# Performance work log

Measured on AMD Instinct MI355X. Metric: run time of the kernel, lower is better.

## Reference

```python
import jax, jax.numpy as jnp
import numpy as np

B, C, IC, H, W = 2, 64, 32, 96, 96


def setup_inputs() -> dict:
    key = jax.random.key(0)
    ks = jax.random.split(key, 8)
    s_in = 1.0 / np.sqrt(C)
    s_ic = 1.0 / np.sqrt(IC)
    return {
        "x": jax.random.normal(ks[0], (B, C, H, W), dtype=jnp.float32),
        "Wg": jax.random.uniform(ks[1], (IC, C), jnp.float32, -s_in, s_in),
        "bg": jax.random.uniform(ks[2], (IC,), jnp.float32, -s_in, s_in),
        "Wt": jax.random.uniform(ks[3], (IC, C), jnp.float32, -s_in, s_in),
        "bt": jax.random.uniform(ks[4], (IC,), jnp.float32, -s_in, s_in),
        "Wp": jax.random.uniform(ks[5], (IC, C), jnp.float32, -s_in, s_in),
        "bp": jax.random.uniform(ks[6], (IC,), jnp.float32, -s_in, s_in),
        "Wo": jax.random.uniform(ks[7], (C, IC), jnp.float32, -s_ic, s_ic),
        "bo": jax.random.uniform(jax.random.fold_in(key, 9), (C,), jnp.float32, -s_ic, s_ic),
    }


def reference(x, Wg, bg, Wt, bt, Wp, bp, Wo, bo):
    b, c, h, w = x.shape
    n = h * w
    xf = x.reshape(b, c, n)  # [B, C, N]

    def proj(Wc, bc):  # 1x1 conv == channel GEMM -> [B, IC, N]
        return jnp.einsum("bcn,oc->bon", xf, Wc) + bc[None, :, None]

    g = proj(Wg, bg)
    theta = proj(Wt, bt)
    phi = proj(Wp, bp)
    scores = jnp.einsum("bcn,bcm->bnm", theta, phi)  # [B, N, N]
    att = jax.nn.softmax(scores, axis=-1)
    y = jnp.einsum("bnm,bcm->bcn", att, g)  # [B, IC, N]
    o = jnp.einsum("bcn,oc->bon", y, Wo) + bo[None, :, None]  # [B, C, N]
    return o.reshape(b, c, h, w) + x
```

## Files before the change

kernel.cpp:

```cpp
#include <hip/hip_runtime.h>
#include <hip/hip_bf16.h>


#define B_   2
#define C_   64
#define IC_  32
#define N_   9216
#define SEG_       8
#define SEG_KEYS   1152
#define SEG_TILES  18
#define QBLKS      144
#define LOG2E 1.44269504088896f

typedef __attribute__((ext_vector_type(4))) float  f32x4;
typedef __attribute__((ext_vector_type(8))) short  s16x8;
typedef __attribute__((ext_vector_type(4))) short  s16x4;

static __device__ __forceinline__ ushort f2bf(float f) {
  union { __hip_bfloat16 h; ushort u; } cv;
  cv.h = __float2bfloat16(f);
  return cv.u;
}

static __device__ __forceinline__ float bf2f(ushort u) {
  union { uint i; float f; } c;
  c.i = ((uint)u) << 16;
  return c.f;
}

static __device__ __forceinline__ f32x4 mfma32(s16x8 a, s16x8 b, f32x4 c) {
  return __builtin_amdgcn_mfma_f32_16x16x32_bf16(a, b, c, 0, 0, 0);
}

__global__ __launch_bounds__(256) void proj_kernel(
    const float* __restrict__ x,
    const float* __restrict__ Wg, const float* __restrict__ bg,
    const float* __restrict__ Wt, const float* __restrict__ bt,
    const float* __restrict__ Wp, const float* __restrict__ bp,
    ushort* __restrict__ Qb, ushort* __restrict__ Kb, ushort* __restrict__ Vt)
{
  const int g    = blockIdx.x / 18;
  const int nblk = blockIdx.x % 18;
  const int bn0  = nblk * 1024 + threadIdx.x * 4;
  const int b    = bn0 / N_;
  const int n    = bn0 % N_;

  float ag[4], at_[4], ap[4];
#pragma unroll
  for (int j = 0; j < 4; ++j) { ag[j] = 0.f; at_[j] = 0.f; ap[j] = 0.f; }

  const float* xp = x + (size_t)b * C_ * N_ + n;
#pragma unroll 8
  for (int c = 0; c < C_; ++c) {
    const f32x4 x0 = *reinterpret_cast<const f32x4*>(xp + (size_t)c * N_);
    const float wg = Wg[g * C_ + c];
    const float wt = Wt[g * C_ + c];
    const float wp = Wp[g * C_ + c];
#pragma unroll
    for (int j = 0; j < 4; ++j) {
      ag[j]  = fmaf(wg, x0[j], ag[j]);
      at_[j] = fmaf(wt, x0[j], at_[j]);
      ap[j]  = fmaf(wp, x0[j], ap[j]);
    }
  }

  const float bgv = bg[g], btv = bt[g], bpv = bp[g];
  union { ushort u[4]; s16x4 v; } vt4;
#pragma unroll
  for (int j = 0; j < 4; ++j) {
    const int bn = bn0 + j;
    Qb[(size_t)bn * IC_ + g] = f2bf(LOG2E * (at_[j] + btv));
    Kb[(size_t)bn * IC_ + g] = f2bf(ap[j] + bpv);
    vt4.u[j] = f2bf(ag[j] + bgv);
  }
  *reinterpret_cast<s16x4*>(Vt + (size_t)(b * IC_ + g) * N_ + n) = vt4.v;
}

__global__ __launch_bounds__(256) void attn_kernel(
    const ushort* __restrict__ Qb, const ushort* __restrict__ Kb,
    const ushort* __restrict__ Vt, ushort* __restrict__ Opart,
    float* __restrict__ Lp)
{
  __shared__ __align__(16) ushort Kl[64 * 40];
  __shared__ __align__(16) ushort Vl[32 * 68];

  const int qblk = blockIdx.x % QBLKS;
  const int bs   = blockIdx.x / QBLKS;
  const int seg  = bs & (SEG_ - 1);
  const int b    = bs >> 3;
  const int key0 = seg * SEG_KEYS;

  const int tid  = threadIdx.x;
  const int lane = tid & 63;
  const int wave = tid >> 6;
  const int q16  = lane & 15;
  const int h    = lane >> 4;

  const int qbase = qblk * 64 + wave * 16;

  const short ONE = (short)0x3F80;
  const s16x8 ones = {ONE, ONE, ONE, ONE, ONE, ONE, ONE, ONE};

  const s16x8 qfrag = *reinterpret_cast<const s16x8*>(
      Qb + (size_t)(b * N_ + qbase + q16) * IC_ + h * 8);

  f32x4 acc0 = {0.f, 0.f, 0.f, 0.f};
  f32x4 acc1 = {0.f, 0.f, 0.f, 0.f};
  f32x4 accL = {0.f, 0.f, 0.f, 0.f};

  const int krow = tid >> 2, kpart = tid & 3;
  const ushort* kg = Kb + ((size_t)b * N_ + key0 + krow) * IC_ + kpart * 8;
  ushort* kl_dst = &Kl[krow * 40 + kpart * 8];

  const int vd0 = tid >> 4, vp = tid & 15;
  const int vd1 = vd0 + 16;
  const ushort* vg0 = Vt + (size_t)(b * IC_ + vd0) * N_ + key0 + vp * 4;
  const ushort* vg1 = Vt + (size_t)(b * IC_ + vd1) * N_ + key0 + vp * 4;
  ushort* vl_dst0 = &Vl[vd0 * 68 + vp * 4];
  ushort* vl_dst1 = &Vl[vd1 * 68 + vp * 4];

  s16x8 kreg = *reinterpret_cast<const s16x8*>(kg);
  s16x4 vreg0 = *reinterpret_cast<const s16x4*>(vg0);
  s16x4 vreg1 = *reinterpret_cast<const s16x4*>(vg1);

  for (int it = 0; it < SEG_TILES; ++it) {
    *reinterpret_cast<s16x8*>(kl_dst)  = kreg;
    *reinterpret_cast<s16x4*>(vl_dst0) = vreg0;
    *reinterpret_cast<s16x4*>(vl_dst1) = vreg1;
    __syncthreads();

    if (it + 1 < SEG_TILES) {
      const int nk = (it + 1) * 64;
      kreg  = *reinterpret_cast<const s16x8*>(kg + (size_t)nk * IC_);
      vreg0 = *reinterpret_cast<const s16x4*>(vg0 + nk);
      vreg1 = *reinterpret_cast<const s16x4*>(vg1 + nk);
    }

    float sc[4][4];
#pragma unroll
    for (int t = 0; t < 4; ++t) {
      const s16x8 kf = *reinterpret_cast<const s16x8*>(&Kl[(t * 16 + q16) * 40 + h * 8]);
      f32x4 z = {0.f, 0.f, 0.f, 0.f};
      const f32x4 st = mfma32(kf, qfrag, z);
      sc[t][0] = st[0]; sc[t][1] = st[1]; sc[t][2] = st[2]; sc[t][3] = st[3];
    }

#pragma unroll
    for (int u = 0; u < 2; ++u) {
      union { ushort us[8]; s16x8 v; } pa;
#pragma unroll
      for (int i = 0; i < 4; ++i) {
        pa.us[i]     = f2bf(__builtin_amdgcn_exp2f(sc[2 * u][i]));
        pa.us[4 + i] = f2bf(__builtin_amdgcn_exp2f(sc[2 * u + 1][i]));
      }
      union { s16x4 q4[2]; s16x8 v; } vf0, vf1;
      vf0.q4[0] = *reinterpret_cast<const s16x4*>(&Vl[q16 * 68 + u * 32 + h * 4]);
      vf0.q4[1] = *reinterpret_cast<const s16x4*>(&Vl[q16 * 68 + u * 32 + 16 + h * 4]);
      vf1.q4[0] = *reinterpret_cast<const s16x4*>(&Vl[(16 + q16) * 68 + u * 32 + h * 4]);
      vf1.q4[1] = *reinterpret_cast<const s16x4*>(&Vl[(16 + q16) * 68 + u * 32 + 16 + h * 4]);
      acc0 = mfma32(pa.v, vf0.v, acc0);
      acc1 = mfma32(pa.v, vf1.v, acc1);
      accL = mfma32(pa.v, ones,  accL);
    }
    __syncthreads();
  }

  const size_t obase0 = ((size_t)(b * SEG_ + seg) * N_);
#pragma unroll
  for (int r = 0; r < 4; ++r) {
    const int q = qbase + h * 4 + r;
    Opart[(obase0 + q) * IC_ + q16]      = f2bf(acc0[r]);
    Opart[(obase0 + q) * IC_ + 16 + q16] = f2bf(acc1[r]);
  }
  if (q16 == 0) {
#pragma unroll
    for (int r = 0; r < 4; ++r)
      Lp[obase0 + qbase + h * 4 + r] = accL[r];
  }
}

__global__ __launch_bounds__(256) void combine_kernel(
    const ushort* __restrict__ Opart, const float* __restrict__ Lp,
    float* __restrict__ Y)
{
  const int idx     = blockIdx.x * 256 + threadIdx.x;
  const int bn      = idx >> 2;
  const int quarter = idx & 3;
  const int b       = bn / N_;
  const int q       = bn % N_;

  float l = 0.f;
  float o[8];
#pragma unroll
  for (int j = 0; j < 8; ++j) o[j] = 0.f;

#pragma unroll
  for (int s = 0; s < SEG_; ++s) {
    const size_t base = (size_t)(b * SEG_ + s) * N_ + q;
    l += Lp[base];
    union { s16x8 v; ushort us[8]; } ov;
    ov.v = *reinterpret_cast<const s16x8*>(Opart + base * IC_ + quarter * 8);
#pragma unroll
    for (int j = 0; j < 8; ++j) o[j] += bf2f(ov.us[j]);
  }
  const float inv = 1.0f / l;
  f32x4 y0 = {o[0] * inv, o[1] * inv, o[2] * inv, o[3] * inv};
  f32x4 y1 = {o[4] * inv, o[5] * inv, o[6] * inv, o[7] * inv};
  f32x4* yp = reinterpret_cast<f32x4*>(Y + (size_t)bn * IC_ + quarter * 8);
  yp[0] = y0; yp[1] = y1;
}

__global__ __launch_bounds__(256) void out_kernel(
    const float* __restrict__ Y, const float* __restrict__ Wo,
    const float* __restrict__ bo, const float* __restrict__ x,
    float* __restrict__ out)
{
  const int g    = blockIdx.x / 72;
  const int nblk = blockIdx.x % 72;
  const int bn   = nblk * 256 + threadIdx.x;
  const int b    = bn / N_;
  const int n    = bn % N_;

  float yv[32];
#pragma unroll
  for (int i = 0; i < 8; ++i) {
    const f32x4 v = *reinterpret_cast<const f32x4*>(Y + (size_t)bn * IC_ + i * 4);
    yv[i * 4 + 0] = v[0]; yv[i * 4 + 1] = v[1];
    yv[i * 4 + 2] = v[2]; yv[i * 4 + 3] = v[3];
  }

  float acc[4];
#pragma unroll
  for (int j = 0; j < 4; ++j) acc[j] = bo[g * 4 + j];

#pragma unroll
  for (int ic = 0; ic < IC_; ++ic) {
    const float yv_ic = yv[ic];
#pragma unroll
    for (int j = 0; j < 4; ++j)
      acc[j] = fmaf(Wo[(g * 4 + j) * IC_ + ic], yv_ic, acc[j]);
  }

#pragma unroll
  for (int j = 0; j < 4; ++j) {
    const int oc = g * 4 + j;
    const size_t xi = (size_t)(b * C_ + oc) * N_ + n;
    out[xi] = acc[j] + x[xi];
  }
}

extern "C" void kernel_launch(void* const* d_in, const int* in_sizes, int n_in,
                              void* d_out, int out_size, void* d_ws, size_t ws_size,
                              hipStream_t stream)
{
  const float* x  = (const float*)d_in[0];
  const float* Wg = (const float*)d_in[1];
  const float* bg = (const float*)d_in[2];
  const float* Wt = (const float*)d_in[3];
  const float* bt = (const float*)d_in[4];
  const float* Wp = (const float*)d_in[5];
  const float* bp = (const float*)d_in[6];
  const float* Wo = (const float*)d_in[7];
  const float* bo = (const float*)d_in[8];
  float* out = (float*)d_out;

  char* ws = (char*)d_ws;
  const size_t szb  = (size_t)B_ * N_ * IC_ * sizeof(ushort);
  const size_t szOp = (size_t)B_ * SEG_ * N_ * IC_ * sizeof(ushort);
  ushort* Qb = (ushort*)(ws);
  ushort* Kb = (ushort*)(ws + szb);
  ushort* Vt = (ushort*)(ws + 2 * szb);
  ushort* Op = (ushort*)(ws + 3 * szb);
  float*  Lp = (float*)(ws + 3 * szb + szOp);
  float*  Yw = (float*)(ws);

  proj_kernel<<<576, 256, 0, stream>>>(x, Wg, bg, Wt, bt, Wp, bp, Qb, Kb, Vt);
  attn_kernel<<<B_ * SEG_ * QBLKS, 256, 0, stream>>>(Qb, Kb, Vt, Op, Lp);
  combine_kernel<<<(B_ * N_ * 4) / 256, 256, 0, stream>>>(Op, Lp, Yw);
  out_kernel<<<16 * 72, 256, 0, stream>>>(Yw, Wo, bo, x, out);
}
```

Measured before the change: 71.75 us.

## Process two query tiles per wave and permute V layout for contiguous LDS reads

The attention kernel now handles 128 queries per block, two 16-query fragments per wave, so each K/V tile staged in LDS is reused twice. The projection kernel writes V in a permuted key order that lets the PV MFMA operand come from one 8-element LDS read instead of two 4-element reads, and computes 8 output channels per thread. The output kernel computes 16 channels per thread, cutting redundant reads of Y. The cost is more registers per thread, fewer blocks, and scattered 2-byte stores in the projection.

```diff
diff --git a/kernel.cpp b/kernel.cpp
--- a/kernel.cpp
+++ b/kernel.cpp
@@ -9,7 +9,7 @@
 #define SEG_       8
 #define SEG_KEYS   1152
 #define SEG_TILES  18
-#define QBLKS      144
+#define QBLK128    72
 #define LOG2E 1.44269504088896f
 
 typedef __attribute__((ext_vector_type(4))) float  f32x4;
@@ -39,53 +39,50 @@
     const float* __restrict__ Wp, const float* __restrict__ bp,
     ushort* __restrict__ Qb, ushort* __restrict__ Kb, ushort* __restrict__ Vt)
 {
-  const int g    = blockIdx.x / 18;
-  const int nblk = blockIdx.x % 18;
-  const int bn0  = nblk * 1024 + threadIdx.x * 4;
-  const int b    = bn0 / N_;
-  const int n    = bn0 % N_;
-
-  float ag[4], at_[4], ap[4];
-#pragma unroll
-  for (int j = 0; j < 4; ++j) { ag[j] = 0.f; at_[j] = 0.f; ap[j] = 0.f; }
+  const int grp = blockIdx.x / 72;
+  const int ic0 = grp * 8;
+  const int bn  = (blockIdx.x % 72) * 256 + threadIdx.x;
+  const int b   = bn / N_;
+  const int n   = bn % N_;
+
+  float ag[8], at_[8], ap[8];
+#pragma unroll
+  for (int j = 0; j < 8; ++j) { ag[j] = 0.f; at_[j] = 0.f; ap[j] = 0.f; }
 
   const float* xp = x + (size_t)b * C_ * N_ + n;
 #pragma unroll 8
   for (int c = 0; c < C_; ++c) {
-    const f32x4 x0 = *reinterpret_cast<const f32x4*>(xp + (size_t)c * N_);
-    const float wg = Wg[g * C_ + c];
-    const float wt = Wt[g * C_ + c];
-    const float wp = Wp[g * C_ + c];
-#pragma unroll
-    for (int j = 0; j < 4; ++j) {
-      ag[j]  = fmaf(wg, x0[j], ag[j]);
-      at_[j] = fmaf(wt, x0[j], at_[j]);
-      ap[j]  = fmaf(wp, x0[j], ap[j]);
-    }
-  }
-
-  const float bgv = bg[g], btv = bt[g], bpv = bp[g];
-  union { ushort u[4]; s16x4 v; } vt4;
-#pragma unroll
-  for (int j = 0; j < 4; ++j) {
-    const int bn = bn0 + j;
-    Qb[(size_t)bn * IC_ + g] = f2bf(LOG2E * (at_[j] + btv));
-    Kb[(size_t)bn * IC_ + g] = f2bf(ap[j] + bpv);
-    vt4.u[j] = f2bf(ag[j] + bgv);
-  }
-  *reinterpret_cast<s16x4*>(Vt + (size_t)(b * IC_ + g) * N_ + n) = vt4.v;
-}
-
-__global__ __launch_bounds__(256) void attn_kernel(
+    const float xv = xp[(size_t)c * N_];
+#pragma unroll
+    for (int j = 0; j < 8; ++j) {
+      ag[j]  = fmaf(Wg[(ic0 + j) * C_ + c], xv, ag[j]);
+      at_[j] = fmaf(Wt[(ic0 + j) * C_ + c], xv, at_[j]);
+      ap[j]  = fmaf(Wp[(ic0 + j) * C_ + c], xv, ap[j]);
+    }
+  }
+
+  const int j6 = n & 63, u = j6 >> 5, r = j6 & 31;
+  const int nperm = (n - j6) + u * 32 + (r & 15) * 2 + (r >> 4);
+
+#pragma unroll
+  for (int j = 0; j < 8; ++j) {
+    const int ic = ic0 + j;
+    Qb[(size_t)bn * IC_ + ic] = f2bf(LOG2E * (at_[j] + bt[ic]));
+    Kb[(size_t)bn * IC_ + ic] = f2bf(ap[j] + bp[ic]);
+    Vt[(size_t)(b * IC_ + ic) * N_ + nperm] = f2bf(ag[j] + bg[ic]);
+  }
+}
+
+__global__ __launch_bounds__(256, 4) void attn_kernel(
     const ushort* __restrict__ Qb, const ushort* __restrict__ Kb,
     const ushort* __restrict__ Vt, ushort* __restrict__ Opart,
     float* __restrict__ Lp)
 {
   __shared__ __align__(16) ushort Kl[64 * 40];
-  __shared__ __align__(16) ushort Vl[32 * 68];
-
-  const int qblk = blockIdx.x % QBLKS;
-  const int bs   = blockIdx.x / QBLKS;
+  __shared__ __align__(16) ushort Vl[32 * 70];
+
+  const int qblk = blockIdx.x % QBLK128;
+  const int bs   = blockIdx.x / QBLK128;
   const int seg  = bs & (SEG_ - 1);
   const int b    = bs >> 3;
   const int key0 = seg * SEG_KEYS;
@@ -96,71 +93,70 @@
   const int q16  = lane & 15;
   const int h    = lane >> 4;
 
-  const int qbase = qblk * 64 + wave * 16;
+  const int qbaseA = qblk * 128 + wave * 32;
+  const int qbaseB = qbaseA + 16;
 
   const short ONE = (short)0x3F80;
   const s16x8 ones = {ONE, ONE, ONE, ONE, ONE, ONE, ONE, ONE};
 
-  const s16x8 qfrag = *reinterpret_cast<const s16x8*>(
-      Qb + (size_t)(b * N_ + qbase + q16) * IC_ + h * 8);
-
-  f32x4 acc0 = {0.f, 0.f, 0.f, 0.f};
-  f32x4 acc1 = {0.f, 0.f, 0.f, 0.f};
-  f32x4 accL = {0.f, 0.f, 0.f, 0.f};
+  const s16x8 qfragA = *reinterpret_cast<const s16x8*>(
+      Qb + (size_t)(b * N_ + qbaseA + q16) * IC_ + h * 8);
+  const s16x8 qfragB = *reinterpret_cast<const s16x8*>(
+      Qb + (size_t)(b * N_ + qbaseB + q16) * IC_ + h * 8);
+
+  f32x4 aA0 = {0.f,0.f,0.f,0.f}, aA1 = {0.f,0.f,0.f,0.f}, aLA = {0.f,0.f,0.f,0.f};
+  f32x4 aB0 = {0.f,0.f,0.f,0.f}, aB1 = {0.f,0.f,0.f,0.f}, aLB = {0.f,0.f,0.f,0.f};
 
   const int krow = tid >> 2, kpart = tid & 3;
   const ushort* kg = Kb + ((size_t)b * N_ + key0 + krow) * IC_ + kpart * 8;
   ushort* kl_dst = &Kl[krow * 40 + kpart * 8];
 
-  const int vd0 = tid >> 4, vp = tid & 15;
-  const int vd1 = vd0 + 16;
-  const ushort* vg0 = Vt + (size_t)(b * IC_ + vd0) * N_ + key0 + vp * 4;
-  const ushort* vg1 = Vt + (size_t)(b * IC_ + vd1) * N_ + key0 + vp * 4;
-  ushort* vl_dst0 = &Vl[vd0 * 68 + vp * 4];
-  ushort* vl_dst1 = &Vl[vd1 * 68 + vp * 4];
+  const int vd = tid >> 3, vp = tid & 7;
+  const ushort* vg = Vt + (size_t)(b * IC_ + vd) * N_ + key0 + vp * 8;
+  ushort* vl_dst = &Vl[vd * 70 + vp * 8];
 
   s16x8 kreg = *reinterpret_cast<const s16x8*>(kg);
-  s16x4 vreg0 = *reinterpret_cast<const s16x4*>(vg0);
-  s16x4 vreg1 = *reinterpret_cast<const s16x4*>(vg1);
+  s16x8 vreg = *reinterpret_cast<const s16x8*>(vg);
 
   for (int it = 0; it < SEG_TILES; ++it) {
-    *reinterpret_cast<s16x8*>(kl_dst)  = kreg;
-    *reinterpret_cast<s16x4*>(vl_dst0) = vreg0;
-    *reinterpret_cast<s16x4*>(vl_dst1) = vreg1;
+    *reinterpret_cast<s16x8*>(kl_dst) = kreg;
+    *reinterpret_cast<s16x8*>(vl_dst) = vreg;
     __syncthreads();
 
     if (it + 1 < SEG_TILES) {
-      const int nk = (it + 1) * 64;
-      kreg  = *reinterpret_cast<const s16x8*>(kg + (size_t)nk * IC_);
-      vreg0 = *reinterpret_cast<const s16x4*>(vg0 + nk);
-      vreg1 = *reinterpret_cast<const s16x4*>(vg1 + nk);
-    }
-
-    float sc[4][4];
-#pragma unroll
-    for (int t = 0; t < 4; ++t) {
-      const s16x8 kf = *reinterpret_cast<const s16x8*>(&Kl[(t * 16 + q16) * 40 + h * 8]);
-      f32x4 z = {0.f, 0.f, 0.f, 0.f};
-      const f32x4 st = mfma32(kf, qfrag, z);
-      sc[t][0] = st[0]; sc[t][1] = st[1]; sc[t][2] = st[2]; sc[t][3] = st[3];
+      kg += 64 * IC_;
+      vg += 64;
+      kreg = *reinterpret_cast<const s16x8*>(kg);
+      vreg = *reinterpret_cast<const s16x8*>(vg);
     }
 
 #pragma unroll
     for (int u = 0; u < 2; ++u) {
-      union { ushort us[8]; s16x8 v; } pa;
+      const s16x8 kf0 = *reinterpret_cast<const s16x8*>(&Kl[(u * 32 + q16) * 40 + h * 8]);
+      const s16x8 kf1 = *reinterpret_cast<const s16x8*>(&Kl[(u * 32 + 16 + q16) * 40 + h * 8]);
+      const f32x4 z = {0.f, 0.f, 0.f, 0.f};
+      const f32x4 sA0 = mfma32(kf0, qfragA, z);
+      const f32x4 sA1 = mfma32(kf1, qfragA, z);
+      const f32x4 sB0 = mfma32(kf0, qfragB, z);
+      const f32x4 sB1 = mfma32(kf1, qfragB, z);
+
+      const s16x8 vf0 = *reinterpret_cast<const s16x8*>(&Vl[q16 * 70 + u * 32 + h * 8]);
+      const s16x8 vf1 = *reinterpret_cast<const s16x8*>(&Vl[(16 + q16) * 70 + u * 32 + h * 8]);
+
+      union { ushort us[8]; s16x8 v; } paA, paB;
 #pragma unroll
       for (int i = 0; i < 4; ++i) {
-        pa.us[i]     = f2bf(__builtin_amdgcn_exp2f(sc[2 * u][i]));
-        pa.us[4 + i] = f2bf(__builtin_amdgcn_exp2f(sc[2 * u + 1][i]));
+        paA.us[2 * i]     = f2bf(__builtin_amdgcn_exp2f(sA0[i]));
+        paA.us[2 * i + 1] = f2bf(__builtin_amdgcn_exp2f(sA1[i]));
+        paB.us[2 * i]     = f2bf(__builtin_amdgcn_exp2f(sB0[i]));
+        paB.us[2 * i + 1] = f2bf(__builtin_amdgcn_exp2f(sB1[i]));
       }
-      union { s16x4 q4[2]; s16x8 v; } vf0, vf1;
-      vf0.q4[0] = *reinterpret_cast<const s16x4*>(&Vl[q16 * 68 + u * 32 + h * 4]);
-      vf0.q4[1] = *reinterpret_cast<const s16x4*>(&Vl[q16 * 68 + u * 32 + 16 + h * 4]);
-      vf1.q4[0] = *reinterpret_cast<const s16x4*>(&Vl[(16 + q16) * 68 + u * 32 + h * 4]);
-      vf1.q4[1] = *reinterpret_cast<const s16x4*>(&Vl[(16 + q16) * 68 + u * 32 + 16 + h * 4]);
-      acc0 = mfma32(pa.v, vf0.v, acc0);
-      acc1 = mfma32(pa.v, vf1.v, acc1);
-      accL = mfma32(pa.v, ones,  accL);
+      aA0 = mfma32(paA.v, vf0, aA0);
+      aA1 = mfma32(paA.v, vf1, aA1);
+      aLA = mfma32(paA.v, ones, aLA);
+      aB0 = mfma32(paB.v, vf0, aB0);
+      aB1 = mfma32(paB.v, vf1, aB1);
+      aLB = mfma32(paB.v, ones, aLB);
     }
     __syncthreads();
   }
@@ -168,14 +164,19 @@
   const size_t obase0 = ((size_t)(b * SEG_ + seg) * N_);
 #pragma unroll
   for (int r = 0; r < 4; ++r) {
-    const int q = qbase + h * 4 + r;
-    Opart[(obase0 + q) * IC_ + q16]      = f2bf(acc0[r]);
-    Opart[(obase0 + q) * IC_ + 16 + q16] = f2bf(acc1[r]);
+    const int qA = qbaseA + h * 4 + r;
+    const int qB = qbaseB + h * 4 + r;
+    Opart[(obase0 + qA) * IC_ + q16]      = f2bf(aA0[r]);
+    Opart[(obase0 + qA) * IC_ + 16 + q16] = f2bf(aA1[r]);
+    Opart[(obase0 + qB) * IC_ + q16]      = f2bf(aB0[r]);
+    Opart[(obase0 + qB) * IC_ + 16 + q16] = f2bf(aB1[r]);
   }
   if (q16 == 0) {
 #pragma unroll
-    for (int r = 0; r < 4; ++r)
-      Lp[obase0 + qbase + h * 4 + r] = accL[r];
+    for (int r = 0; r < 4; ++r) {
+      Lp[obase0 + qbaseA + h * 4 + r] = aLA[r];
+      Lp[obase0 + qbaseB + h * 4 + r] = aLB[r];
+    }
   }
 }
 
@@ -216,8 +217,8 @@
     float* __restrict__ out)
 {
   const int g    = blockIdx.x / 72;
-  const int nblk = blockIdx.x % 72;
-  const int bn   = nblk * 256 + threadIdx.x;
+  const int oc0  = g * 16;
+  const int bn   = (blockIdx.x % 72) * 256 + threadIdx.x;
   const int b    = bn / N_;
   const int n    = bn % N_;
 
@@ -229,21 +230,21 @@
     yv[i * 4 + 2] = v[2]; yv[i * 4 + 3] = v[3];
   }
 
-  float acc[4];
-#pragma unroll
-  for (int j = 0; j < 4; ++j) acc[j] = bo[g * 4 + j];
+  float acc[16];
+#pragma unroll
+  for (int j = 0; j < 16; ++j) acc[j] = bo[oc0 + j];
 
 #pragma unroll
   for (int ic = 0; ic < IC_; ++ic) {
     const float yv_ic = yv[ic];
 #pragma unroll
-    for (int j = 0; j < 4; ++j)
-      acc[j] = fmaf(Wo[(g * 4 + j) * IC_ + ic], yv_ic, acc[j]);
-  }
-
-#pragma unroll
-  for (int j = 0; j < 4; ++j) {
-    const int oc = g * 4 + j;
+    for (int j = 0; j < 16; ++j)
+      acc[j] = fmaf(Wo[(oc0 + j) * IC_ + ic], yv_ic, acc[j]);
+  }
+
+#pragma unroll
+  for (int j = 0; j < 16; ++j) {
+    const int oc = oc0 + j;
     const size_t xi = (size_t)(b * C_ + oc) * N_ + n;
     out[xi] = acc[j] + x[xi];
   }
@@ -274,8 +275,8 @@
   float*  Lp = (float*)(ws + 3 * szb + szOp);
   float*  Yw = (float*)(ws);
 
-  proj_kernel<<<576, 256, 0, stream>>>(x, Wg, bg, Wt, bt, Wp, bp, Qb, Kb, Vt);
-  attn_kernel<<<B_ * SEG_ * QBLKS, 256, 0, stream>>>(Qb, Kb, Vt, Op, Lp);
+  proj_kernel<<<288, 256, 0, stream>>>(x, Wg, bg, Wt, bt, Wp, bp, Qb, Kb, Vt);
+  attn_kernel<<<B_ * SEG_ * QBLK128, 256, 0, stream>>>(Qb, Kb, Vt, Op, Lp);
   combine_kernel<<<(B_ * N_ * 4) / 256, 256, 0, stream>>>(Op, Lp, Yw);
-  out_kernel<<<16 * 72, 256, 0, stream>>>(Yw, Wo, bo, x, out);
-}
+  out_kernel<<<4 * 72, 256, 0, stream>>>(Yw, Wo, bo, x, out);
+}
```

After: 75.30 us. +4.9%, slower.
